# Optimization experiments

Measured on AMD Instinct MI355X. Metric: run time of the kernel, lower is better.

## Reference

```python
import jax, jax.numpy as jnp
import numpy as np

# opt constants baked from init_kwargs
OPT_M = 1024      # number of OFDM subcarriers (opt.M)
N_PILOT = 0       # opt.N_pilot
VELOCITY = 100.0  # opt.V (is_random_v=False)
DECAY = 4.0       # opt.decay
C_LIGHT = 3.0e8
CARRIER_FREQ = 3.0e9


def setup_inputs() -> dict:
    key = jax.random.key(0)
    k1, k2 = jax.random.split(key, 2)
    N, P, L, M, S = 16, 4, 16, OPT_M, 128
    # channel tap power profile: exp(-l/decay), normalized
    power = jnp.exp(-jnp.arange(L, dtype=jnp.float32) / DECAY)
    power = power / jnp.sum(power)
    # Rayleigh(sigma=1) samples = sqrt(g1^2 + g2^2), g_i ~ N(0,1)
    g = jax.random.normal(k1, (N, P, L, 2), dtype=jnp.float32)
    rayleigh = jnp.sqrt(g[..., 0] ** 2 + g[..., 1] ** 2)
    cof = jnp.sqrt(power / 2.0) * rayleigh  # (N,P,L), strictly positive
    input_ri = jax.random.normal(k2, (N, P, S * M, 2), dtype=jnp.float32)
    return {"input_ri": input_ri, "cof": cof, "Ns": 128}


def reference(input_ri, cof, Ns):
    N, P, SMK, _ = input_ri.shape
    L = cof.shape[-1]
    S = Ns + N_PILOT  # OFDM mode: S = Ns + N_pilot, M = opt.M
    Mk = SMK // S
    x = (input_ri[..., 0] + 1j * input_ri[..., 1]).astype(jnp.complex64)  # (N,P,SMK)

    # per-tap propagation delay from tap gain: len = -100*log(cof); delay1 = len/c
    delay1 = (-100.0 * jnp.log(cof)) / C_LIGHT                      # (N,P,L)
    delay2 = jnp.linspace(0.0, (S - 1) * (0.0005 / 14.0), S).astype(jnp.float32)  # (S,)
    delay = delay1[..., None] + delay2                              # (N,P,L,S)

    max_doppler = VELOCITY / C_LIGHT * CARRIER_FREQ
    angles = jnp.linspace(0.0, 2.0 * np.pi, L).astype(jnp.float32)  # (L,)
    phase_coef = (2.0 * np.pi * jnp.cos(angles) * max_doppler)      # (L,)
    phases = phase_coef[None, None, :, None] * delay                # (N,P,L,S)
    shift = jnp.exp(-1j * phases.astype(jnp.float32))               # complex64 (N,P,L,S)

    # sum over taps L BEFORE multiplying by the L-independent input (same math,
    # avoids materializing the (N,P,L,S,M) broadcast intermediate)
    factor = jnp.sum(cof[..., None].astype(jnp.complex64) * shift, axis=2)  # (N,P,S)
    out = x.reshape(N, P, S, Mk) * factor[..., None]                # (N,P,S,M)
    out = out.reshape(N, P, SMK)
    out_ri = jnp.stack([out.real, out.imag], axis=-1)               # (N,P,SMK,2)

    # frequency response H_t = FFT of zero-padded taps
    cof_zp = jnp.concatenate([cof, jnp.zeros((N, P, OPT_M - L), cof.dtype)], axis=-1)
    H_t = jnp.fft.fft(cof_zp.astype(jnp.complex64), axis=-1)        # (N,P,OPT_M)
    H_t_ri = jnp.stack([H_t.real, H_t.imag], axis=-1)
    return out_ri, H_t_ri
```

## Files before the change

### kernel.cpp

```cpp
#include <hip/hip_runtime.h>
#include <math.h>

#define NB     16
#define PB     4
#define LTAPS  16
#define SS     128
#define MM     1024

#define TWO_PI_F 6.28318530717958647692f

#define FAC_BLKS  32
#define HT_BLKS   256

__global__ __launch_bounds__(256) void small_kernel(
    const float* __restrict__ cof,
    float* __restrict__ fac,
    float* __restrict__ ht)
{
    const int b = blockIdx.x;
    const int t = threadIdx.x;

    if (b < FAC_BLKS) {
        const int id = b * 256 + t;
        const int np = id >> 7;
        const int s  = id & (SS - 1);
        const float delay2 = (0.0005f / 14.0f) * (float)s;
        float fre = 0.0f, fim = 0.0f;
#pragma unroll
        for (int l = 0; l < LTAPS; ++l) {
            const float cofl   = cof[np * LTAPS + l];
            const float delay1 = (-100.0f / 3.0e8f) * logf(cofl);
            const float angle  = (TWO_PI_F / 15.0f) * (float)l;
            const float pc     = TWO_PI_F * cosf(angle) * 1000.0f;
            const float ph     = pc * (delay1 + delay2);
            float sn, cs;
            sincosf(ph, &sn, &cs);
            fre += cofl * cs;
            fim -= cofl * sn;
        }
        ((float2*)fac)[id] = make_float2(fre, fim);
    } else {
        const int id = (b - FAC_BLKS) * 256 + t;
        const int np = id >> 10;
        const int k  = id & (MM - 1);
        float re = 0.0f, im = 0.0f;
#pragma unroll
        for (int l = 0; l < LTAPS; ++l) {
            const float ang = (TWO_PI_F / (float)MM) * (float)(k * l);
            float sn, cs;
            sincosf(ang, &sn, &cs);
            const float c = cof[np * LTAPS + l];
            re += c * cs;
            im -= c * sn;
        }
        ((float2*)ht)[id] = make_float2(re, im);
    }
}

#define TOT4 (NB * PB * SS * MM / 2)

__global__ __launch_bounds__(256) void main_kernel(
    const float* __restrict__ in,
    const float* __restrict__ fac,
    float* __restrict__ out)
{
    const float2* __restrict__ f2 = (const float2*)fac;
    const float4* __restrict__ in4 = (const float4*)in;
    float4* __restrict__ out4 = (float4*)out;

    const int stride = gridDim.x * 256;
    for (int g = blockIdx.x * 256 + threadIdx.x; g < TOT4; g += stride) {
        const float2 f = f2[g >> 9];
        const float4 v = in4[g];
        float4 r;
        r.x = v.x * f.x - v.y * f.y;
        r.y = v.x * f.y + v.y * f.x;
        r.z = v.z * f.x - v.w * f.y;
        r.w = v.z * f.y + v.w * f.x;
        out4[g] = r;
    }
}

extern "C" void kernel_launch(void* const* d_in, const int* in_sizes, int n_in,
                              void* d_out, int out_size, void* d_ws, size_t ws_size,
                              hipStream_t stream)
{
    const float* in  = (const float*)d_in[0];
    const float* cof = (const float*)d_in[1];
    float* out = (float*)d_out;
    float* ht  = out + (size_t)NB * PB * SS * MM * 2;
    float* fac = (float*)d_ws;

    hipLaunchKernelGGL(small_kernel, dim3(FAC_BLKS + HT_BLKS), dim3(256), 0, stream,
                       cof, fac, ht);
    hipLaunchKernelGGL(main_kernel, dim3(2048), dim3(256), 0, stream,
                       in, fac, out);
}
```

Measured before the change: 30.86 us.

## Fuse factor computation into streaming kernel and use twiddle recurrence for H_t

Merges the two launches into one kernel. Each streaming block recomputes the 8 per-(n,p,s) factors it needs in shared memory, using 128 threads that each handle one tap, then streams its input/output chunks. This removes the second launch, the inter-kernel dependency and the workspace round trip. The H_t branch swaps 16 sincos calls per output for a single sincos plus a complex-multiply recurrence, which may slightly change rounding. Every streaming block now spends redundant transcendental work and two block barriers before it starts streaming.

```diff
diff --git a/kernel.cpp b/kernel.cpp
--- a/kernel.cpp
+++ b/kernel.cpp
@@ -9,75 +9,86 @@
 
 #define TWO_PI_F 6.28318530717958647692f
 
-#define FAC_BLKS  32
-#define HT_BLKS   256
+#define STREAM_BLKS 2048
+#define HT_BLKS     256
+#define TOT4 (NB * PB * SS * MM / 2)
 
-__global__ __launch_bounds__(256) void small_kernel(
+__global__ __launch_bounds__(256) void fused_kernel(
+    const float* __restrict__ in,
     const float* __restrict__ cof,
-    float* __restrict__ fac,
+    float* __restrict__ out,
     float* __restrict__ ht)
 {
     const int b = blockIdx.x;
     const int t = threadIdx.x;
 
-    if (b < FAC_BLKS) {
-        const int id = b * 256 + t;
-        const int np = id >> 7;
-        const int s  = id & (SS - 1);
-        const float delay2 = (0.0005f / 14.0f) * (float)s;
-        float fre = 0.0f, fim = 0.0f;
-#pragma unroll
-        for (int l = 0; l < LTAPS; ++l) {
+    if (b < STREAM_BLKS) {
+        __shared__ float term_re[128], term_im[128];
+        __shared__ float2 facs[8];
+
+        const int base = b >> 1;
+        if (t < 128) {
+            const int k  = t >> 4;
+            const int l  = t & 15;
+            const int id = base + k * 1024;
+            const int np = id >> 7;
+            const int s  = id & (SS - 1);
             const float cofl   = cof[np * LTAPS + l];
             const float delay1 = (-100.0f / 3.0e8f) * logf(cofl);
-            const float angle  = (TWO_PI_F / 15.0f) * (float)l;
-            const float pc     = TWO_PI_F * cosf(angle) * 1000.0f;
+            const float delay2 = (0.0005f / 14.0f) * (float)s;
+            const float pc     = TWO_PI_F * 1000.0f * cosf((TWO_PI_F / 15.0f) * (float)l);
             const float ph     = pc * (delay1 + delay2);
             float sn, cs;
             sincosf(ph, &sn, &cs);
-            fre += cofl * cs;
-            fim -= cofl * sn;
+            term_re[t] = cofl * cs;
+            term_im[t] = -cofl * sn;
         }
-        ((float2*)fac)[id] = make_float2(fre, fim);
+        __syncthreads();
+        if (t < 8) {
+            float re = 0.0f, im = 0.0f;
+#pragma unroll
+            for (int l = 0; l < LTAPS; ++l) {
+                re += term_re[t * 16 + l];
+                im += term_im[t * 16 + l];
+            }
+            facs[t] = make_float2(re, im);
+        }
+        __syncthreads();
+
+        const float4* __restrict__ in4  = (const float4*)in;
+        float4* __restrict__       out4 = (float4*)out;
+        int g = b * 256 + t;
+#pragma unroll
+        for (int k = 0; k < 8; ++k, g += STREAM_BLKS * 256) {
+            const float2 f = facs[k];
+            const float4 v = in4[g];
+            float4 r;
+            r.x = v.x * f.x - v.y * f.y;
+            r.y = v.x * f.y + v.y * f.x;
+            r.z = v.z * f.x - v.w * f.y;
+            r.w = v.z * f.y + v.w * f.x;
+            out4[g] = r;
+        }
     } else {
-        const int id = (b - FAC_BLKS) * 256 + t;
+        const int id = (b - STREAM_BLKS) * 256 + t;
         const int np = id >> 10;
         const int k  = id & (MM - 1);
-        float re = 0.0f, im = 0.0f;
+        float sn, cs;
+        sincosf((TWO_PI_F / (float)MM) * (float)k, &sn, &cs);
+        const float wr = cs, wi = -sn;
+        const float* __restrict__ c = cof + np * LTAPS;
+        float hr = 0.0f, hi = 0.0f;
+        float cr = 1.0f, ci = 0.0f;
 #pragma unroll
         for (int l = 0; l < LTAPS; ++l) {
-            const float ang = (TWO_PI_F / (float)MM) * (float)(k * l);
-            float sn, cs;
-            sincosf(ang, &sn, &cs);
-            const float c = cof[np * LTAPS + l];
-            re += c * cs;
-            im -= c * sn;
+            const float cl = c[l];
+            hr += cl * cr;
+            hi += cl * ci;
+            const float nr = cr * wr - ci * wi;
+            const float ni = cr * wi + ci * wr;
+            cr = nr; ci = ni;
         }
-        ((float2*)ht)[id] = make_float2(re, im);
-    }
-}
-
-#define TOT4 (NB * PB * SS * MM / 2)
-
-__global__ __launch_bounds__(256) void main_kernel(
-    const float* __restrict__ in,
-    const float* __restrict__ fac,
-    float* __restrict__ out)
-{
-    const float2* __restrict__ f2 = (const float2*)fac;
-    const float4* __restrict__ in4 = (const float4*)in;
-    float4* __restrict__ out4 = (float4*)out;
-
-    const int stride = gridDim.x * 256;
-    for (int g = blockIdx.x * 256 + threadIdx.x; g < TOT4; g += stride) {
-        const float2 f = f2[g >> 9];
-        const float4 v = in4[g];
-        float4 r;
-        r.x = v.x * f.x - v.y * f.y;
-        r.y = v.x * f.y + v.y * f.x;
-        r.z = v.z * f.x - v.w * f.y;
-        r.w = v.z * f.y + v.w * f.x;
-        out4[g] = r;
+        ((float2*)ht)[id] = make_float2(hr, hi);
     }
 }
 
@@ -89,10 +100,7 @@
     const float* cof = (const float*)d_in[1];
     float* out = (float*)d_out;
     float* ht  = out + (size_t)NB * PB * SS * MM * 2;
-    float* fac = (float*)d_ws;
 
-    hipLaunchKernelGGL(small_kernel, dim3(FAC_BLKS + HT_BLKS), dim3(256), 0, stream,
-                       cof, fac, ht);
-    hipLaunchKernelGGL(main_kernel, dim3(2048), dim3(256), 0, stream,
-                       in, fac, out);
+    hipLaunchKernelGGL(fused_kernel, dim3(STREAM_BLKS + HT_BLKS), dim3(256), 0, stream,
+                       in, cof, out, ht);
 }
```

New measurement: 28.66 us. 1.08x faster.
